# Optimization experiments

Measured on AMD Instinct MI355X. Metric: run time of the kernel, lower is better.

## Reference

```python
import jax, jax.numpy as jnp
import numpy as np

B, S, D = 4, 2048, 1024
H, K = 16, 64
EPS = 1e-3  # Keras LayerNormalization default epsilon


def setup_inputs() -> dict:
    key = jax.random.key(0)
    ks = jax.random.split(key, 11)
    s = 0.02
    return {
        "x":  jax.random.normal(ks[0], (B, S, D), jnp.float32),
        "Wq": jax.random.normal(ks[1], (D, H, K), jnp.float32) * s,
        "bq": jnp.zeros((H, K), jnp.float32),
        "Wk": jax.random.normal(ks[2], (D, H, K), jnp.float32) * s,
        "bk": jnp.zeros((H, K), jnp.float32),
        "Wv": jax.random.normal(ks[3], (D, H, K), jnp.float32) * s,
        "bv": jnp.zeros((H, K), jnp.float32),
        "Wo": jax.random.normal(ks[4], (H, K, D), jnp.float32) * s,
        "bo": jnp.zeros((D,), jnp.float32),
        "gamma": jnp.ones((D,), jnp.float32),
        "beta":  jnp.zeros((D,), jnp.float32),
    }


def reference(x, Wq, bq, Wk, bk, Wv, bv, Wo, bo, gamma, beta):
    # QKV projections (Keras MHA einsum form): [B,S,D] -> [B,S,H,K]
    q = jnp.einsum("bsd,dhk->bshk", x, Wq) + bq
    k = jnp.einsum("bsd,dhk->bshk", x, Wk) + bk
    v = jnp.einsum("bsd,dhk->bshk", x, Wv) + bv
    scale = 1.0 / jnp.sqrt(jnp.asarray(K, x.dtype))
    scores = jnp.einsum("bqhk,bshk->bhqs", q, k) * scale  # [B,H,S,S]
    attn = jax.nn.softmax(scores, axis=-1)
    ctx = jnp.einsum("bhqs,bshk->bqhk", attn, v)           # [B,S,H,K]
    attn_out = jnp.einsum("bqhk,hkd->bqd", ctx, Wo) + bo   # [B,S,D]
    # residual + LayerNorm (over last axis)
    y = x + attn_out
    mu = jnp.mean(y, axis=-1, keepdims=True)
    var = jnp.mean(jnp.square(y - mu), axis=-1, keepdims=True)
    return (y - mu) * jax.lax.rsqrt(var + EPS) * gamma + beta
```

## Files before the change

### kernel.cpp

```cpp
#include <hip/hip_runtime.h>

typedef float f32x4 __attribute__((ext_vector_type(4)));
typedef float f32x16 __attribute__((ext_vector_type(16)));
typedef __bf16 bf16x8 __attribute__((ext_vector_type(8)));
typedef __bf16 bf16x4 __attribute__((ext_vector_type(4)));
typedef __bf16 bf16x2 __attribute__((ext_vector_type(2)));
typedef unsigned short us4 __attribute__((ext_vector_type(4)));

#define DEV __device__ __forceinline__

DEV unsigned short f2bf(float f) {
  union { float f; unsigned int u; } v; v.f = f;
  unsigned int u = v.u;
  return (unsigned short)((u + 0x7FFFu + ((u >> 16) & 1u)) >> 16);
}

typedef const __attribute__((address_space(1))) void* gvp;
typedef __attribute__((address_space(3))) void* lvp;

DEV void gll16(const void* g, void* l) {
  __builtin_amdgcn_global_load_lds((gvp)g, (lvp)l, 16, 0, 0);
}

DEV float fexp2(float x) { return __builtin_amdgcn_exp2f(x); }

DEV void plswap(unsigned& a, unsigned& b) {
  asm("v_permlane32_swap_b32 %0, %1" : "+v"(a), "+v"(b));
}
DEV float xhalf_sum(float v) {
  union { float f; unsigned u; } a, b;
  a.f = v; b.f = v;
  plswap(a.u, b.u);
  return a.f + b.f;
}

__global__ void k_pre(const float* __restrict__ x, unsigned short* __restrict__ xb,
                      const float* __restrict__ w0, const float* __restrict__ w1,
                      const float* __restrict__ w2, const float* __restrict__ w3,
                      unsigned short* __restrict__ o0, unsigned short* __restrict__ o1,
                      unsigned short* __restrict__ o2, unsigned short* __restrict__ o3) {
  __shared__ float tile[32][33];
  const int bid = blockIdx.x;
  const int tid = threadIdx.x;
  if (bid < 8192) {
    int i = bid * 256 + tid;
    float4 v = ((const float4*)x)[i];
    us4 o = { f2bf(v.x), f2bf(v.y), f2bf(v.z), f2bf(v.w) };
    ((us4*)xb)[i] = o;
    return;
  }
  int t = bid - 8192;
  const int z = t >> 10;
  t &= 1023;
  const float* in = (z == 0) ? w0 : (z == 1) ? w1 : (z == 2) ? w2 : w3;
  unsigned short* out = (z == 0) ? o0 : (z == 1) ? o1 : (z == 2) ? o2 : o3;
  const int bx = (t & 31) * 32, by = (t >> 5) * 32;
  const int tx = tid & 31, ty = tid >> 5;
#pragma unroll
  for (int r = 0; r < 4; ++r)
    tile[ty + r * 8][tx] = in[(size_t)(by + ty + r * 8) * 1024 + bx + tx];
  __syncthreads();
#pragma unroll
  for (int r = 0; r < 4; ++r)
    out[(size_t)(bx + ty + r * 8) * 1024 + by + tx] = f2bf(tile[tx][ty + r * 8]);
}

__global__ void k_gemm_qkv(const unsigned short* __restrict__ xb,
                           const unsigned short* __restrict__ wqt,
                           const unsigned short* __restrict__ wkt,
                           const unsigned short* __restrict__ wvt,
                           const float* __restrict__ bq, const float* __restrict__ bk,
                           const float* __restrict__ bv,
                           unsigned short* __restrict__ qb, unsigned short* __restrict__ kb,
                           unsigned short* __restrict__ vtb) {
  __shared__ unsigned short SM[2][128 * 64];
  unsigned short* As = SM[0];
  unsigned short* Bs = SM[1];
  const int tid = threadIdx.x;
  const int lane = tid & 63;
  const int wave = tid >> 6;
  const int l15 = lane & 15;
  const int lq  = lane >> 4;
  const int wm = wave >> 1, wn = wave & 1;
  const int z = blockIdx.z;

  const unsigned short* A;
  const unsigned short* Bt;
  int mbase, nbase;
  if (z == 2) { A = wvt; Bt = xb; mbase = blockIdx.y * 128; nbase = blockIdx.x * 128; }
  else        { A = xb; Bt = z ? wkt : wqt; mbase = blockIdx.x * 128; nbase = blockIdx.y * 128; }

  f32x4 acc[4][4] = {};

  for (int kt = 0; kt < 1024; kt += 64) {
    __syncthreads();
#pragma unroll
    for (int c = 0; c < 4; ++c) {
      int e = (c * 256 + tid) * 8;
      int row = e >> 6;
      int o2 = (e * 2) ^ ((row & 7) << 4);
      int col = (o2 >> 1) & 63;
      gll16(A + (size_t)(mbase + row) * 1024 + kt + col,
            As + (c * 256 + (tid & ~63)) * 8);
      gll16(Bt + (size_t)(nbase + row) * 1024 + kt + col,
            Bs + (c * 256 + (tid & ~63)) * 8);
    }
    __syncthreads();
#pragma unroll
    for (int ks = 0; ks < 2; ++ks) {
      bf16x8 af[4], bfv[4];
#pragma unroll
      for (int i = 0; i < 4; ++i) {
        int row = wm * 64 + i * 16 + l15;
        int off = row * 128 + ((((ks << 2) | lq) ^ (row & 7)) << 4);
        af[i] = *(const bf16x8*)((const char*)As + off);
      }
#pragma unroll
      for (int j = 0; j < 4; ++j) {
        int row = wn * 64 + j * 16 + l15;
        int off = row * 128 + ((((ks << 2) | lq) ^ (row & 7)) << 4);
        bfv[j] = *(const bf16x8*)((const char*)Bs + off);
      }
#pragma unroll
      for (int i = 0; i < 4; ++i)
#pragma unroll
        for (int j = 0; j < 4; ++j)
          acc[i][j] = __builtin_amdgcn_mfma_f32_16x16x32_bf16(bfv[j], af[i], acc[i][j], 0, 0, 0);
    }
  }

  const float scale = (z == 0) ? 0.18033688011112042f : 1.0f;
  const float* bias = (z == 0) ? bq : (z == 1) ? bk : bv;
  unsigned short* outp = (z == 0) ? qb : (z == 1) ? kb : vtb;

  float4 bj[4];
  if (z < 2) {
#pragma unroll
    for (int j = 0; j < 4; ++j)
      bj[j] = *(const float4*)&bias[nbase + wn * 64 + j * 16 + lq * 4];
  }

  __syncthreads();
  char* T = (char*)SM;
#pragma unroll
  for (int i = 0; i < 4; ++i) {
    const int miL = wm * 64 + i * 16 + l15;
    const int sw = (miL & 7) << 4;
    const float bm = (z == 2) ? bias[mbase + miL] : 0.f;
#pragma unroll
    for (int j = 0; j < 4; ++j) {
      const int nj2 = (wn * 64 + j * 16 + lq * 4) * 2;
      bf16x4 p;
#pragma unroll
      for (int r = 0; r < 4; ++r) {
        float v = acc[i][j][r];
        v = (z < 2) ? (v + ((const float*)&bj[j])[r]) * scale : (v + bm);
        p[r] = (__bf16)v;
      }
      *(bf16x4*)(T + miL * 256 + (nj2 ^ sw)) = p;
    }
  }
  __syncthreads();

#pragma unroll
  for (int c = 0; c < 8; ++c) {
    const int lin = c * 256 + tid;
    const int row = lin >> 4;
    const int s16 = lin & 15;
    bf16x8 vv = *(const bf16x8*)(T + row * 256 + ((s16 * 16) ^ ((row & 7) << 4)));
    const int mi = mbase + row;
    const int nj = nbase + s16 * 8;
    size_t gaddr;
    if (z < 2) {
      gaddr = (((size_t)((mi >> 11) * 16 + (nj >> 6)) * 2048 + (mi & 2047)) << 6) + (nj & 63);
    } else {
      gaddr = ((size_t)(((nj >> 11) * 16 + (mi >> 6)) * 64 + (mi & 63))) * 2048 + (nj & 2047);
    }
    *(bf16x8*)(outp + gaddr) = vv;
  }
}

__global__ void k_gemm_out(const unsigned short* __restrict__ A,
                           const unsigned short* __restrict__ Bt,
                           const float* __restrict__ bias,
                           unsigned short* __restrict__ yb,
                           const unsigned short* __restrict__ xres) {
  __shared__ unsigned short SMo[2][128 * 64];
  unsigned short* As = SMo[0];
  unsigned short* Bs = SMo[1];
  const int tid = threadIdx.x;
  const int lane = tid & 63;
  const int wave = tid >> 6;
  const int l15 = lane & 15;
  const int lq  = lane >> 4;
  const int wm = wave >> 1, wn = wave & 1;
  const int mbase = blockIdx.x * 128;
  const int nbase = blockIdx.y * 128;

  f32x4 acc[4][4] = {};

  for (int kt = 0; kt < 1024; kt += 64) {
    __syncthreads();
#pragma unroll
    for (int c = 0; c < 4; ++c) {
      int e = (c * 256 + tid) * 8;
      int row = e >> 6;
      int o2 = (e * 2) ^ ((row & 7) << 4);
      int col = (o2 >> 1) & 63;
      gll16(A + (size_t)(mbase + row) * 1024 + kt + col,
            As + (c * 256 + (tid & ~63)) * 8);
      gll16(Bt + (size_t)(nbase + row) * 1024 + kt + col,
            Bs + (c * 256 + (tid & ~63)) * 8);
    }
    __syncthreads();
#pragma unroll
    for (int ks = 0; ks < 2; ++ks) {
      bf16x8 af[4], bfv[4];
#pragma unroll
      for (int i = 0; i < 4; ++i) {
        int row = wm * 64 + i * 16 + l15;
        int off = row * 128 + ((((ks << 2) | lq) ^ (row & 7)) << 4);
        af[i] = *(const bf16x8*)((const char*)As + off);
      }
#pragma unroll
      for (int j = 0; j < 4; ++j) {
        int row = wn * 64 + j * 16 + l15;
        int off = row * 128 + ((((ks << 2) | lq) ^ (row & 7)) << 4);
        bfv[j] = *(const bf16x8*)((const char*)Bs + off);
      }
#pragma unroll
      for (int i = 0; i < 4; ++i)
#pragma unroll
        for (int j = 0; j < 4; ++j)
          acc[i][j] = __builtin_amdgcn_mfma_f32_16x16x32_bf16(bfv[j], af[i], acc[i][j], 0, 0, 0);
    }
  }

  float4 bj[4];
#pragma unroll
  for (int j = 0; j < 4; ++j)
    bj[j] = *(const float4*)&bias[nbase + wn * 64 + j * 16 + lq * 4];

  __syncthreads();
  char* T = (char*)SMo;
#pragma unroll
  for (int i = 0; i < 4; ++i) {
    const int miL = wm * 64 + i * 16 + l15;
    const int sw = (miL & 7) << 4;
#pragma unroll
    for (int j = 0; j < 4; ++j) {
      const int nj2 = (wn * 64 + j * 16 + lq * 4) * 2;
      bf16x4 p;
#pragma unroll
      for (int r = 0; r < 4; ++r)
        p[r] = (__bf16)(acc[i][j][r] + ((const float*)&bj[j])[r]);
      *(bf16x4*)(T + miL * 256 + (nj2 ^ sw)) = p;
    }
  }
  __syncthreads();

#pragma unroll
  for (int c = 0; c < 8; ++c) {
    const int lin = c * 256 + tid;
    const int row = lin >> 4;
    const int s16 = lin & 15;
    bf16x8 vv = *(const bf16x8*)(T + row * 256 + ((s16 * 16) ^ ((row & 7) << 4)));
    const size_t g = (size_t)(mbase + row) * 1024 + nbase + s16 * 8;
    bf16x8 xv = *(const bf16x8*)(xres + g);
    bf16x8 ov;
#pragma unroll
    for (int e = 0; e < 8; ++e)
      ov[e] = (__bf16)((float)vv[e] + (float)xv[e]);
    *(bf16x8*)(yb + g) = ov;
  }
}

__global__ __launch_bounds__(256, 4) void k_attn(const unsigned short* __restrict__ q,
                       const unsigned short* __restrict__ k,
                       const unsigned short* __restrict__ vt,
                       unsigned short* __restrict__ ctx) {
  __shared__ unsigned short KL[3][64 * 64];
  __shared__ unsigned short VL[2][64 * 64];

  const int tid = threadIdx.x;
  const int lane = tid & 63;
  const int wave = tid >> 6;
  const int l31 = lane & 31;
  const int l5 = lane >> 5;
  const int prl = l31 >> 1;
  const int b3  = (l31 & 1) << 3;

  const int bid = blockIdx.x;
  const int swz = (bid & 7) * 128 + (bid >> 3);
  const int bh = swz >> 4;
  const int qtile = swz & 15;
  const int qbase = qtile * 128;
  const size_t sl = (size_t)bh << 17;

  const int qrow = qbase + wave * 32 + l31;
  bf16x8 qreg[4];
#pragma unroll
  for (int ds = 0; ds < 4; ++ds)
    qreg[ds] = *(const bf16x8*)(q + sl + (size_t)qrow * 64 + ds * 16 + l5 * 8);

#define STAGE_K(DST, TT) do {                                                  \
    const int kvb_ = (TT) * 64;                                                \
    _Pragma("unroll")                                                          \
    for (int c = 0; c < 2; ++c) {                                              \
      int ci = c * 256 + tid;                                                  \
      int pr_ = ci >> 4;                                                       \
      int u_ = (ci & 15) ^ (pr_ & 15);                                         \
      int lrow_ = pr_ * 2 + (u_ >> 3);                                         \
      int lc_ = u_ & 7;                                                        \
      gll16(k + sl + (size_t)(kvb_ + lrow_) * 64 + lc_ * 8,                    \
            (DST) + (c * 256 + (tid & ~63)) * 8);                              \
    }                                                                          \
  } while (0)
#define STAGE_V(DST, TT) do {                                                  \
    const int kvb_ = (TT) * 64;                                                \
    _Pragma("unroll")                                                          \
    for (int c = 0; c < 2; ++c) {                                              \
      int ci = c * 256 + tid;                                                  \
      int pr_ = ci >> 4;                                                       \
      int u_ = (ci & 15) ^ (pr_ & 15);                                         \
      int lrow_ = pr_ * 2 + (u_ >> 3);                                         \
      int lc_ = u_ & 7;                                                        \
      gll16(vt + sl + (size_t)lrow_ * 2048 + kvb_ + lc_ * 8,                   \
            (DST) + (c * 256 + (tid & ~63)) * 8);                              \
    }                                                                          \
  } while (0)

  STAGE_K(KL[0], 0);
  STAGE_V(VL[0], 0);
  STAGE_K(KL[1], 1);

  f32x16 acc0 = {}, acc1 = {};
  float lrow = 0.f;

  for (int t = 0; t < 32; ++t) {
    asm volatile("s_waitcnt vmcnt(2)" ::: "memory");
    __builtin_amdgcn_s_barrier();

    const char* Ksc = (const char*)KL[t % 3];
    const char* Vtc = (const char*)VL[t & 1];

    bf16x8 kf0[4], kf1[4];
#pragma unroll
    for (int ds = 0; ds < 4; ++ds) {
      int sc = (b3 | (2 * ds + l5)) ^ prl;
      kf0[ds] = *(const bf16x8*)(Ksc + prl * 256 + sc * 16);
      kf1[ds] = *(const bf16x8*)(Ksc + 4096 + prl * 256 + sc * 16);
    }
    f32x16 s0 = {}, s1 = {};
    __builtin_amdgcn_s_setprio(1);
#pragma unroll
    for (int ds = 0; ds < 4; ++ds)
      s0 = __builtin_amdgcn_mfma_f32_32x32x16_bf16(kf0[ds], qreg[ds], s0, 0, 0, 0);
#pragma unroll
    for (int ds = 0; ds < 4; ++ds)
      s1 = __builtin_amdgcn_mfma_f32_32x32x16_bf16(kf1[ds], qreg[ds], s1, 0, 0, 0);
    __builtin_amdgcn_s_setprio(0);

    {
      const int tv = (t + 1 < 32) ? t + 1 : 31;
      STAGE_V(VL[(t + 1) & 1], tv);
    }
    __builtin_amdgcn_sched_barrier(0);

    unsigned pk0[8], pk1[8];
    float r0s = 0.f, r1s = 0.f, r2s = 0.f, r3s = 0.f;
#pragma unroll
    for (int m = 0; m < 8; ++m) {
      float a0 = fexp2(s0[2 * m]), a1 = fexp2(s0[2 * m + 1]);
      float b0 = fexp2(s1[2 * m]), b1 = fexp2(s1[2 * m + 1]);
      r0s += a0; r1s += a1; r2s += b0; r3s += b1;
      union { bf16x2 v; unsigned u; } ua, ub;
      ua.v = bf16x2{ (__bf16)a0, (__bf16)a1 };
      ub.v = bf16x2{ (__bf16)b0, (__bf16)b1 };
      pk0[m] = ua.u; pk1[m] = ub.u;
    }
    lrow += (r0s + r1s) + (r2s + r3s);
    __builtin_amdgcn_sched_barrier(0);

    bf16x8 av0[4], av1[4];
#pragma unroll
    for (int kvg = 0; kvg < 4; ++kvg) {
      int sc = (b3 | (2 * kvg + l5)) ^ prl;
      av0[kvg] = *(const bf16x8*)(Vtc + prl * 256 + sc * 16);
      av1[kvg] = *(const bf16x8*)(Vtc + 4096 + prl * 256 + sc * 16);
    }
    __builtin_amdgcn_s_setprio(1);
#pragma unroll
    for (int kvh = 0; kvh < 2; ++kvh) {
      unsigned* pk = kvh ? pk1 : pk0;
#pragma unroll
      for (int g = 0; g < 2; ++g) {
        unsigned a0_ = pk[4 * g],     b0_ = pk[4 * g + 2];
        unsigned a1_ = pk[4 * g + 1], b1_ = pk[4 * g + 3];
        plswap(a0_, b0_);
        plswap(a1_, b1_);
        union { unsigned u[4]; bf16x8 v; } pf;
        pf.u[0] = a0_; pf.u[1] = a1_; pf.u[2] = b0_; pf.u[3] = b1_;
        const int kvg = 2 * kvh + g;
        acc0 = __builtin_amdgcn_mfma_f32_32x32x16_bf16(av0[kvg], pf.v, acc0, 0, 0, 0);
        acc1 = __builtin_amdgcn_mfma_f32_32x32x16_bf16(av1[kvg], pf.v, acc1, 0, 0, 0);
      }
    }
    __builtin_amdgcn_s_setprio(0);

    {
      const int tk = (t + 2 < 32) ? t + 2 : 31;
      STAGE_K(KL[(t + 2) % 3], tk);
    }
  }

  const float inv = 1.f / xhalf_sum(lrow);

  __syncthreads();
  unsigned short* TR = (unsigned short*)KL;
  const int qloc = wave * 32 + l31;
  const int swq = (qloc & 7) << 4;
#pragma unroll
  for (int dh = 0; dh < 2; ++dh) {
    const f32x16& ac = dh ? acc1 : acc0;
#pragma unroll
    for (int g3 = 0; g3 < 4; ++g3) {
      bf16x4 o4 = { (__bf16)(ac[4 * g3] * inv), (__bf16)(ac[4 * g3 + 1] * inv),
                    (__bf16)(ac[4 * g3 + 2] * inv), (__bf16)(ac[4 * g3 + 3] * inv) };
      *(bf16x4*)((char*)TR + qloc * 128 + ((dh * 64 + g3 * 16 + l5 * 8) ^ swq)) = o4;
    }
  }
  __syncthreads();

  const int b = bh >> 4, h = bh & 15;
  {
    int row = tid >> 1, half = tid & 1;
    int sw = (row & 7) << 4;
    unsigned short* gdst = ctx + (size_t)(b * 2048 + qbase + row) * 1024 + h * 64 + half * 32;
#pragma unroll
    for (int i = 0; i < 4; ++i) {
      bf16x8 vv = *(const bf16x8*)((const char*)TR + row * 128 + ((half * 64 + i * 16) ^ sw));
      *(bf16x8*)(gdst + i * 8) = vv;
    }
  }
#undef STAGE_K
#undef STAGE_V
}

__global__ void k_ln(const unsigned short* __restrict__ y, const float* __restrict__ gamma,
                     const float* __restrict__ beta, float* __restrict__ out) {
  const int row = blockIdx.x;
  const int tid = threadIdx.x;
  const bf16x4 v4 = *(const bf16x4*)(y + (size_t)row * 1024 + tid * 4);
  float v0 = (float)v4[0], v1 = (float)v4[1], v2 = (float)v4[2], v3 = (float)v4[3];
  float sum = v0 + v1 + v2 + v3;
  float sq = v0 * v0 + v1 * v1 + v2 * v2 + v3 * v3;
#pragma unroll
  for (int m = 1; m <= 32; m <<= 1) {
    sum += __shfl_xor(sum, m);
    sq  += __shfl_xor(sq, m);
  }
  __shared__ float s1[4], s2[4];
  const int wv = tid >> 6, lane = tid & 63;
  if (lane == 0) { s1[wv] = sum; s2[wv] = sq; }
  __syncthreads();
  sum = s1[0] + s1[1] + s1[2] + s1[3];
  sq  = s2[0] + s2[1] + s2[2] + s2[3];
  const float mu = sum * (1.f / 1024.f);
  const float rs = rsqrtf(sq * (1.f / 1024.f) - mu * mu + 1e-3f);
  const float4 g  = ((const float4*)gamma)[tid];
  const float4 bb = ((const float4*)beta)[tid];
  float4 o;
  o.x = (v0 - mu) * rs * g.x + bb.x;
  o.y = (v1 - mu) * rs * g.y + bb.y;
  o.z = (v2 - mu) * rs * g.z + bb.z;
  o.w = (v3 - mu) * rs * g.w + bb.w;
  ((float4*)(out + (size_t)row * 1024))[tid] = o;
}

extern "C" void kernel_launch(void* const* d_in, const int* in_sizes, int n_in,
                              void* d_out, int out_size, void* d_ws, size_t ws_size,
                              hipStream_t stream) {
  const float* x  = (const float*)d_in[0];
  const float* Wq = (const float*)d_in[1];
  const float* bq = (const float*)d_in[2];
  const float* Wk = (const float*)d_in[3];
  const float* bk = (const float*)d_in[4];
  const float* Wv = (const float*)d_in[5];
  const float* bv = (const float*)d_in[6];
  const float* Wo = (const float*)d_in[7];
  const float* bo = (const float*)d_in[8];
  const float* gamma = (const float*)d_in[9];
  const float* beta  = (const float*)d_in[10];
  float* out = (float*)d_out;

  char* ws = (char*)d_ws;
  const size_t MB = 1024 * 1024;
  unsigned short* xb  = (unsigned short*)(ws);
  unsigned short* wqt = (unsigned short*)(ws + 16 * MB);
  unsigned short* wkt = (unsigned short*)(ws + 18 * MB);
  unsigned short* wvt = (unsigned short*)(ws + 20 * MB);
  unsigned short* wot = (unsigned short*)(ws + 22 * MB);
  unsigned short* qb  = (unsigned short*)(ws + 24 * MB);
  unsigned short* kb  = (unsigned short*)(ws + 40 * MB);
  unsigned short* vtb = (unsigned short*)(ws + 56 * MB);
  unsigned short* ctx = (unsigned short*)(ws + 72 * MB);
  unsigned short* yb  = (unsigned short*)(ws + 24 * MB);

  k_pre<<<12288, 256, 0, stream>>>(x, xb, Wq, Wk, Wv, Wo, wqt, wkt, wvt, wot);

  k_gemm_qkv<<<dim3(64, 8, 3), 256, 0, stream>>>(xb, wqt, wkt, wvt, bq, bk, bv, qb, kb, vtb);

  k_attn<<<1024, 256, 0, stream>>>(qb, kb, vtb, ctx);

  k_gemm_out<<<dim3(64, 8), 256, 0, stream>>>(ctx, wot, bo, yb, xb);

  k_ln<<<8192, 256, 0, stream>>>(yb, gamma, beta, out);
  (void)in_sizes; (void)n_in; (void)out_size; (void)ws_size;
}
```

Before: 183.8 us.

## Software-pipeline attention loop so QK of the next tile overlaps PV of the previous

Restructures the attention main loop so each iteration computes QK^T for tile t, then PV for tile t-1, then exp/packing for tile t. Probabilities live in ping-pong register sets. Buffers change to double-buffered K and triple-buffered V, with a prologue and epilogue. The aim is to let the exp/softmax ALU work and the MFMA work from different tiles overlap instead of serialising. In exchange, the old explicit vmcnt(2) wait becomes a plain __syncthreads, which may shrink prefetch depth, and the extra live probability registers add register pressure.

Result: slower. 481.7 us (+162.1%).

```diff
diff --git a/kernel.cpp b/kernel.cpp
--- a/kernel.cpp
+++ b/kernel.cpp
@@ -279,8 +279,8 @@
                        const unsigned short* __restrict__ k,
                        const unsigned short* __restrict__ vt,
                        unsigned short* __restrict__ ctx) {
-  __shared__ unsigned short KL[3][64 * 64];
-  __shared__ unsigned short VL[2][64 * 64];
+  __shared__ unsigned short KL[2][64 * 64];
+  __shared__ unsigned short VL[3][64 * 64];
 
   const int tid = threadIdx.x;
   const int lane = tid & 63;
@@ -303,7 +303,7 @@
   for (int ds = 0; ds < 4; ++ds)
     qreg[ds] = *(const bf16x8*)(q + sl + (size_t)qrow * 64 + ds * 16 + l5 * 8);
 
-#define STAGE_K(DST, TT) do {                                                  \
+#define STAGE_K(BUFI, TT) do {                                                 \
     const int kvb_ = (TT) * 64;                                                \
     _Pragma("unroll")                                                          \
     for (int c = 0; c < 2; ++c) {                                              \
@@ -313,10 +313,10 @@
       int lrow_ = pr_ * 2 + (u_ >> 3);                                         \
       int lc_ = u_ & 7;                                                        \
       gll16(k + sl + (size_t)(kvb_ + lrow_) * 64 + lc_ * 8,                    \
-            (DST) + (c * 256 + (tid & ~63)) * 8);                              \
+            KL[BUFI] + (c * 256 + (tid & ~63)) * 8);                           \
     }                                                                          \
   } while (0)
-#define STAGE_V(DST, TT) do {                                                  \
+#define STAGE_V(BUFI, TT) do {                                                 \
     const int kvb_ = (TT) * 64;                                                \
     _Pragma("unroll")                                                          \
     for (int c = 0; c < 2; ++c) {                                              \
@@ -326,95 +326,107 @@
       int lrow_ = pr_ * 2 + (u_ >> 3);                                         \
       int lc_ = u_ & 7;                                                        \
       gll16(vt + sl + (size_t)lrow_ * 2048 + kvb_ + lc_ * 8,                   \
-            (DST) + (c * 256 + (tid & ~63)) * 8);                              \
+            VL[BUFI] + (c * 256 + (tid & ~63)) * 8);                           \
     }                                                                          \
   } while (0)
 
-  STAGE_K(KL[0], 0);
-  STAGE_V(VL[0], 0);
-  STAGE_K(KL[1], 1);
-
   f32x16 acc0 = {}, acc1 = {};
-  float lrow = 0.f;
-
-  for (int t = 0; t < 32; ++t) {
-    asm volatile("s_waitcnt vmcnt(2)" ::: "memory");
-    __builtin_amdgcn_s_barrier();
-
-    const char* Ksc = (const char*)KL[t % 3];
-    const char* Vtc = (const char*)VL[t & 1];
-
-    bf16x8 kf0[4], kf1[4];
-#pragma unroll
-    for (int ds = 0; ds < 4; ++ds) {
-      int sc = (b3 | (2 * ds + l5)) ^ prl;
-      kf0[ds] = *(const bf16x8*)(Ksc + prl * 256 + sc * 16);
-      kf1[ds] = *(const bf16x8*)(Ksc + 4096 + prl * 256 + sc * 16);
-    }
-    f32x16 s0 = {}, s1 = {};
-    __builtin_amdgcn_s_setprio(1);
-#pragma unroll
-    for (int ds = 0; ds < 4; ++ds)
-      s0 = __builtin_amdgcn_mfma_f32_32x32x16_bf16(kf0[ds], qreg[ds], s0, 0, 0, 0);
-#pragma unroll
-    for (int ds = 0; ds < 4; ++ds)
-      s1 = __builtin_amdgcn_mfma_f32_32x32x16_bf16(kf1[ds], qreg[ds], s1, 0, 0, 0);
-    __builtin_amdgcn_s_setprio(0);
-
-    {
-      const int tv = (t + 1 < 32) ? t + 1 : 31;
-      STAGE_V(VL[(t + 1) & 1], tv);
-    }
-    __builtin_amdgcn_sched_barrier(0);
-
-    unsigned pk0[8], pk1[8];
-    float r0s = 0.f, r1s = 0.f, r2s = 0.f, r3s = 0.f;
-#pragma unroll
-    for (int m = 0; m < 8; ++m) {
-      float a0 = fexp2(s0[2 * m]), a1 = fexp2(s0[2 * m + 1]);
-      float b0 = fexp2(s1[2 * m]), b1 = fexp2(s1[2 * m + 1]);
-      r0s += a0; r1s += a1; r2s += b0; r3s += b1;
-      union { bf16x2 v; unsigned u; } ua, ub;
-      ua.v = bf16x2{ (__bf16)a0, (__bf16)a1 };
-      ub.v = bf16x2{ (__bf16)b0, (__bf16)b1 };
-      pk0[m] = ua.u; pk1[m] = ub.u;
-    }
-    lrow += (r0s + r1s) + (r2s + r3s);
-    __builtin_amdgcn_sched_barrier(0);
-
-    bf16x8 av0[4], av1[4];
-#pragma unroll
-    for (int kvg = 0; kvg < 4; ++kvg) {
-      int sc = (b3 | (2 * kvg + l5)) ^ prl;
-      av0[kvg] = *(const bf16x8*)(Vtc + prl * 256 + sc * 16);
-      av1[kvg] = *(const bf16x8*)(Vtc + 4096 + prl * 256 + sc * 16);
-    }
-    __builtin_amdgcn_s_setprio(1);
-#pragma unroll
-    for (int kvh = 0; kvh < 2; ++kvh) {
-      unsigned* pk = kvh ? pk1 : pk0;
-#pragma unroll
-      for (int g = 0; g < 2; ++g) {
-        unsigned a0_ = pk[4 * g],     b0_ = pk[4 * g + 2];
-        unsigned a1_ = pk[4 * g + 1], b1_ = pk[4 * g + 3];
-        plswap(a0_, b0_);
-        plswap(a1_, b1_);
-        union { unsigned u[4]; bf16x8 v; } pf;
-        pf.u[0] = a0_; pf.u[1] = a1_; pf.u[2] = b0_; pf.u[3] = b1_;
-        const int kvg = 2 * kvh + g;
-        acc0 = __builtin_amdgcn_mfma_f32_32x32x16_bf16(av0[kvg], pf.v, acc0, 0, 0, 0);
-        acc1 = __builtin_amdgcn_mfma_f32_32x32x16_bf16(av1[kvg], pf.v, acc1, 0, 0, 0);
-      }
-    }
-    __builtin_amdgcn_s_setprio(0);
-
-    {
-      const int tk = (t + 2 < 32) ? t + 2 : 31;
-      STAGE_K(KL[(t + 2) % 3], tk);
-    }
-  }
-
-  const float inv = 1.f / xhalf_sum(lrow);
+  const f32x16 vzero = {};
+  f32x16 s0, s1;
+  float lr0 = 0.f, lr1 = 0.f, lr2 = 0.f, lr3 = 0.f;
+  unsigned pkA0[8], pkA1[8], pkB0[8], pkB1[8];
+
+#define QK(TT) do {                                                            \
+    const char* Ksc_ = (const char*)KL[(TT) & 1];                              \
+    bf16x8 kf0[4], kf1[4];                                                     \
+    _Pragma("unroll")                                                          \
+    for (int ds = 0; ds < 4; ++ds) {                                           \
+      int sc = (b3 | (2 * ds + l5)) ^ prl;                                     \
+      kf0[ds] = *(const bf16x8*)(Ksc_ + prl * 256 + sc * 16);                  \
+      kf1[ds] = *(const bf16x8*)(Ksc_ + 4096 + prl * 256 + sc * 16);           \
+    }                                                                          \
+    s0 = vzero; s1 = vzero;                                                    \
+    __builtin_amdgcn_s_setprio(1);                                             \
+    _Pragma("unroll")                                                          \
+    for (int ds = 0; ds < 4; ++ds)                                             \
+      s0 = __builtin_amdgcn_mfma_f32_32x32x16_bf16(kf0[ds], qreg[ds], s0, 0, 0, 0); \
+    _Pragma("unroll")                                                          \
+    for (int ds = 0; ds < 4; ++ds)                                             \
+      s1 = __builtin_amdgcn_mfma_f32_32x32x16_bf16(kf1[ds], qreg[ds], s1, 0, 0, 0); \
+    __builtin_amdgcn_s_setprio(0);                                             \
+  } while (0)
+
+#define SMAX(P0, P1) do {                                                      \
+    _Pragma("unroll")                                                          \
+    for (int m = 0; m < 8; ++m) {                                              \
+      float a0 = fexp2(s0[2 * m]), a1 = fexp2(s0[2 * m + 1]);                  \
+      float b0 = fexp2(s1[2 * m]), b1 = fexp2(s1[2 * m + 1]);                  \
+      lr0 += a0; lr1 += a1; lr2 += b0; lr3 += b1;                              \
+      union { bf16x2 v; unsigned u; } ua, ub;                                  \
+      ua.v = bf16x2{ (__bf16)a0, (__bf16)a1 };                                 \
+      ub.v = bf16x2{ (__bf16)b0, (__bf16)b1 };                                 \
+      P0[m] = ua.u; P1[m] = ub.u;                                              \
+    }                                                                          \
+  } while (0)
+
+#define PV(P0, P1, VBUFI) do {                                                 \
+    const char* Vtc_ = (const char*)VL[VBUFI];                                 \
+    bf16x8 av0[4], av1[4];                                                     \
+    _Pragma("unroll")                                                          \
+    for (int kvg = 0; kvg < 4; ++kvg) {                                        \
+      int sc = (b3 | (2 * kvg + l5)) ^ prl;                                    \
+      av0[kvg] = *(const bf16x8*)(Vtc_ + prl * 256 + sc * 16);                 \
+      av1[kvg] = *(const bf16x8*)(Vtc_ + 4096 + prl * 256 + sc * 16);          \
+    }                                                                          \
+    _Pragma("unroll")                                                          \
+    for (int kvh = 0; kvh < 2; ++kvh) {                                        \
+      unsigned* pk_ = kvh ? (P1) : (P0);                                       \
+      _Pragma("unroll")                                                        \
+      for (int g = 0; g < 2; ++g) {                                            \
+        unsigned a0_ = pk_[4 * g],     b0_ = pk_[4 * g + 2];                   \
+        unsigned a1_ = pk_[4 * g + 1], b1_ = pk_[4 * g + 3];                   \
+        plswap(a0_, b0_);                                                      \
+        plswap(a1_, b1_);                                                      \
+        union { unsigned u[4]; bf16x8 v; } pf;                                 \
+        pf.u[0] = a0_; pf.u[1] = a1_; pf.u[2] = b0_; pf.u[3] = b1_;            \
+        const int kvg = 2 * kvh + g;                                           \
+        acc0 = __builtin_amdgcn_mfma_f32_32x32x16_bf16(av0[kvg], pf.v, acc0, 0, 0, 0); \
+        acc1 = __builtin_amdgcn_mfma_f32_32x32x16_bf16(av1[kvg], pf.v, acc1, 0, 0, 0); \
+      }                                                                        \
+    }                                                                          \
+  } while (0)
+
+#define BODY(TT, PKW0, PKW1, PKR0, PKR1) do {                                  \
+    __syncthreads();                                                           \
+    QK(TT);                                                                    \
+    if ((TT) < 31) {                                                           \
+      STAGE_K(((TT) + 1) & 1, (TT) + 1);                                       \
+      STAGE_V(((TT) + 1) % 3, (TT) + 1);                                       \
+    }                                                                          \
+    __builtin_amdgcn_sched_barrier(0);                                         \
+    PV(PKR0, PKR1, ((TT) - 1) % 3);                                            \
+    SMAX(PKW0, PKW1);                                                          \
+    __builtin_amdgcn_sched_barrier(0);                                         \
+  } while (0)
+
+  STAGE_K(0, 0);
+  STAGE_V(0, 0);
+  __syncthreads();
+  QK(0);
+  STAGE_K(1, 1);
+  STAGE_V(1, 1);
+  __builtin_amdgcn_sched_barrier(0);
+  SMAX(pkB0, pkB1);
+  __builtin_amdgcn_sched_barrier(0);
+
+  for (int tp = 1; tp < 31; tp += 2) {
+    BODY(tp,     pkA0, pkA1, pkB0, pkB1);
+    BODY(tp + 1, pkB0, pkB1, pkA0, pkA1);
+  }
+  BODY(31, pkA0, pkA1, pkB0, pkB1);
+  PV(pkA0, pkA1, 31 % 3);
+
+  const float inv = 1.f / xhalf_sum(((lr0 + lr1) + (lr2 + lr3)));
 
   __syncthreads();
   unsigned short* TR = (unsigned short*)KL;
@@ -445,6 +457,10 @@
   }
 #undef STAGE_K
 #undef STAGE_V
+#undef QK
+#undef SMAX
+#undef PV
+#undef BODY
 }
 
 __global__ void k_ln(const unsigned short* __restrict__ y, const float* __restrict__ gamma,
```
